# Kernel tuning notes

Measured on AMD Instinct MI355X. Metric: run time of the kernel, lower is better.

## Reference

```python
import jax, jax.numpy as jnp
import numpy as np

NEG = -1e30  # safe -inf surrogate (avoids nan grads through where)
NUM_CLASSES = 128
BLANK = NUM_CLASSES - 1
B, T, L = 256, 512, 64


def setup_inputs() -> dict:
    key = jax.random.key(0)
    k1, k2, k3, k4 = jax.random.split(key, 4)
    y_pred = jax.random.normal(k1, (B, T, NUM_CLASSES), dtype=jnp.float32)
    y_true = jax.random.randint(k2, (B, L), 0, BLANK, dtype=jnp.int32)  # labels in [0, C-2]
    input_length = jax.random.randint(k3, (B,), T // 2, T + 1, dtype=jnp.int32)
    label_length = jax.random.randint(k4, (B,), L // 2, L + 1, dtype=jnp.int32)
    return {"y_true": y_true, "y_pred": y_pred,
            "input_length": input_length, "label_length": label_length}


def ctc_loss(y_pred, y_true, input_length, label_length):
    # y_pred: [B,T,C] logits (batch-major), y_true: [B,L] int labels, blank = C-1.
    Bs, Ts, C = y_pred.shape
    Ls = y_true.shape[1]
    S = 2 * Ls + 1  # extended label lattice: blank, l1, blank, l2, ..., blank
    lp = jax.nn.log_softmax(y_pred.astype(jnp.float32), axis=-1)  # [B,T,C]
    z = jnp.full((Bs, S), BLANK, dtype=jnp.int32).at[:, 1::2].set(y_true)  # [B,S]
    idx = jnp.broadcast_to(z[:, None, :], (Bs, Ts, S))
    lp_z = jnp.take_along_axis(lp, idx, axis=2)  # [B,T,S] log p(z_s | t)
    # skip transition s-2 -> s allowed when z_s is a label differing from z_{s-2}
    s_idx = jnp.arange(S)
    z_m2 = jnp.pad(z[:, :-2], ((0, 0), (2, 0)), constant_values=BLANK)
    skip = (s_idx[None, :] >= 2) & (z != BLANK) & (z != z_m2)  # [B,S]
    alpha0 = (jnp.full((Bs, S), NEG, jnp.float32)
              .at[:, 0].set(lp_z[:, 0, 0])
              .at[:, 1].set(lp_z[:, 0, 1]))
    lps = jnp.moveaxis(lp_z[:, 1:, :], 1, 0)  # [T-1, B, S]
    ts = jnp.arange(1, Ts)

    def step(alpha, xs):
        t, lpt = xs
        a1 = jnp.pad(alpha[:, :-1], ((0, 0), (1, 0)), constant_values=NEG)
        a2 = jnp.where(skip, jnp.pad(alpha[:, :-2], ((0, 0), (2, 0)), constant_values=NEG), NEG)
        new = jnp.logaddexp(jnp.logaddexp(alpha, a1), a2) + lpt
        # freeze rows whose sequence already ended (t >= input_length)
        alpha = jnp.where((t < input_length)[:, None], new, alpha)
        return alpha, None

    alphaT, _ = jax.lax.scan(step, alpha0, (ts, lps))
    e1 = (2 * label_length)[:, None]  # final blank position per row
    a_end = jnp.take_along_axis(alphaT, e1, axis=1)[:, 0]
    a_end2 = jnp.take_along_axis(alphaT, e1 - 1, axis=1)[:, 0]
    return -jnp.logaddexp(a_end, a_end2)  # [B] negative log-likelihood


def reference(y_true, y_pred, input_length, label_length):
    # tf.nn.ctc_loss(labels, logits, label_length, logit_length,
    #                logits_time_major=False, blank_index=num_classes-1)
    return ctc_loss(y_pred, y_true, input_length, label_length)
```

## Files before the change

kernel.cpp:

```cpp
#include <hip/hip_runtime.h>
#include <hip/hip_fp16.h>
#include <math.h>


constexpr int Cc = 128;
constexpr int Tt = 512;
constexpr int Ll = 64;
constexpr int NCH = Tt / 8;
constexpr int NPW = 15;
constexpr int NR  = (NCH + NPW - 1) / NPW;
constexpr float INV_LN2 = 1.4426950408889634f;
constexpr float LN2_F   = 0.6931471805599453f;

__device__ __forceinline__ float fexp2(float x) { return __builtin_amdgcn_exp2f(x); }
__device__ __forceinline__ float flog2(float x) { return __builtin_amdgcn_logf(x); }

template<int CTRL, bool BC>
__device__ __forceinline__ float dppf(float old, float x) {
    return __int_as_float(__builtin_amdgcn_update_dpp(
        __float_as_int(old), __float_as_int(x), CTRL, 0xF, 0xF, BC));
}
__device__ __forceinline__ float wshr1(float x, float fill) { return dppf<0x138, false>(fill, x); }

__device__ __forceinline__ float rlf(float v, int lane) {
    return __int_as_float(__builtin_amdgcn_readlane(__float_as_int(v), lane));
}
__device__ __forceinline__ float rowsum(float e) {
    e += dppf<0x111, true>(0.f, e);
    e += dppf<0x112, true>(0.f, e);
    e += dppf<0x114, true>(0.f, e);
    e += dppf<0x118, true>(0.f, e);
    return e;
}
__device__ __forceinline__ float rowmax(float m) {
    m = fmaxf(m, dppf<0x111, true>(0.f, m));
    m = fmaxf(m, dppf<0x112, true>(0.f, m));
    m = fmaxf(m, dppf<0x114, true>(0.f, m));
    m = fmaxf(m, dppf<0x118, true>(0.f, m));
    return m;
}
__device__ __forceinline__ float allmax(float m) {
    m = rowmax(m);
    return fmaxf(fmaxf(rlf(m, 15), rlf(m, 31)), fmaxf(rlf(m, 47), rlf(m, 63)));
}
__device__ __forceinline__ float bperm_f(int srclane, float v) {
    return __int_as_float(__builtin_amdgcn_ds_bpermute(srclane << 2, __float_as_int(v)));
}
__device__ __forceinline__ float gather4(float4 v, int srclane, int csel) {
    const float gx = bperm_f(srclane, v.x), gy = bperm_f(srclane, v.y);
    const float gz = bperm_f(srclane, v.z), gw = bperm_f(srclane, v.w);
    const float lo = (csel & 1) ? gy : gx;
    const float hi = (csel & 1) ? gw : gz;
    return (csel & 2) ? hi : lo;
}

template<bool GUARD>
__device__ __forceinline__ void do_chunk(uint4 raw, int t0, int inlen, float skf,
                                         float& aO, float& aE, float& r0, float& Rtot)
{
    float dv[8];
    {
        const __half2 h0 = *reinterpret_cast<const __half2*>(&raw.x);
        const __half2 h1 = *reinterpret_cast<const __half2*>(&raw.y);
        const __half2 h2 = *reinterpret_cast<const __half2*>(&raw.z);
        const __half2 h3 = *reinterpret_cast<const __half2*>(&raw.w);
        dv[0] = __low2float(h0); dv[1] = __high2float(h0);
        dv[2] = __low2float(h1); dv[3] = __high2float(h1);
        dv[4] = __low2float(h2); dv[5] = __high2float(h2);
        dv[6] = __low2float(h3); dv[7] = __high2float(h3);
    }
    float sd[8];
#pragma unroll
    for (int j = 0; j < 8; ++j) sd[j] = skf * dv[j];
#pragma unroll
    for (int j = 0; j < 8; ++j) {
        if (!GUARD || (t0 + j < inlen)) {
            const float ad = aO * dv[j];
            const float pE = wshr1(aE, r0);
            const float pO = wshr1(aO, 0.0f);
            const float nO = fmaf(pE, dv[j], fmaf(pO, sd[j], ad));
            aE += aO;
            aO = nO;
        }
    }
    const float M_ = allmax(fmaxf(fmaxf(aO, aE), r0));
    int R_ = (int)(__float_as_uint(M_) >> 23) - 127;
    R_ = (R_ < 0) ? 0 : ((R_ > 126) ? 126 : R_);
    const float sc = __uint_as_float((unsigned)(127 - R_) << 23);
    aO = fminf(aO * sc, 4.0f);
    aE = fminf(aE * sc, 4.0f);
    r0 = fminf(r0 * sc, 4.0f);
    Rtot += (float)R_;
}

__global__ __launch_bounds__(1024, 1) void ctc_fused4_kernel(
    const int* __restrict__ y_true,
    const float* __restrict__ y_pred,
    const int* __restrict__ in_len,
    const int* __restrict__ lab_len,
    float* __restrict__ out)
{
    __shared__ __half w_lds[NCH][64][8];
    __shared__ float  ps[NPW];
    __shared__ int    rctr[NR];

    const int b   = blockIdx.x;
    const int tid = threadIdx.x;
    const int w   = tid >> 6;
    const int l   = tid & 63;

    if (tid < NR) rctr[tid] = 0;
    __syncthreads();

    int inlen = in_len[b]; if (inlen < 1) inlen = 1; if (inlen > Tt) inlen = Tt;
    int LLv   = lab_len[b]; if (LLv < 1) LLv = 1; if (LLv > Ll) LLv = Ll;

    const int lab = y_true[b * Ll + l] & 127;
    const float* rowbase = y_pred + (size_t)b * Tt * Cc;

    if (w != 0) {
        const int pw   = w - 1;
        const int half = l >> 5, li = l & 31;
        const int srcA = lab >> 2;
        const int csel = lab & 3;
        const bool live = (l < LLv);

        float acc = 0.0f;

        float4 vb[4];
#pragma unroll
        for (int j = 0; j < 4; ++j)
            vb[j] = ((const float4*)(rowbase + (size_t)(pw * 8 + 2 * j + half) * Cc))[li];

        int r = 0;
        for (int c = pw; c < NCH; c += NPW, ++r) {
            const int cn = (c + NPW < NCH) ? (c + NPW) : (NCH - 1);
            float prod = 1.0f, bsum = 0.0f;
#pragma unroll
            for (int j = 0; j < 4; ++j) {
                const float4 v = vb[j];
                vb[j] = ((const float4*)(rowbase + (size_t)(cn * 8 + 2 * j + half) * Cc))[li];

                const int rA = c * 8 + 2 * j;
                const int rB = rA + 1;

                float e = (fexp2(v.x * INV_LN2) + fexp2(v.y * INV_LN2))
                        + (fexp2(v.z * INV_LN2) + fexp2(v.w * INV_LN2));
                e = rowsum(e);
                const float sA = rlf(e, 15) + rlf(e, 31);
                const float sB = rlf(e, 47) + rlf(e, 63);
                const float blA = rlf(v.w, 31);
                const float blB = rlf(v.w, 63);

                const bool okA = rA < inlen, okB = rB < inlen;
                prod *= okB ? sA * sB : (okA ? sA : 1.0f);
                bsum += okB ? blA + blB : (okA ? blA : 0.0f);

                const float xA = gather4(v, srcA, csel);
                const float xB = gather4(v, srcA + 32, csel);
                float wA = fminf(fmaxf(fexp2((xA - blA) * INV_LN2), 6.1e-5f), 8192.0f);
                float wB = fminf(fmaxf(fexp2((xB - blB) * INV_LN2), 6.1e-5f), 8192.0f);
                wA = live ? wA : 0.0f;
                wB = live ? wB : 0.0f;
                const unsigned packed =
                      (unsigned)__half_as_ushort(__float2half(wA))
                    | ((unsigned)__half_as_ushort(__float2half(wB)) << 16);
                *(unsigned*)&w_lds[c][l][2 * j] = packed;
            }
            acc = fmaf(bsum, INV_LN2, acc) - flog2(prod);
            if (c + NPW >= NCH && l == 0) ps[pw] = acc;
            asm volatile("s_waitcnt lgkmcnt(0)" ::: "memory");
            if (l == 0) atomicAdd(&rctr[r], 1);
        }
        return;
    }

    const int labp = __shfl_up(lab, 1, 64);
    const float skf = ((l >= 1) && (lab != labp)) ? 1.0f : 0.0f;

    float aO = 0.0f, aE = 0.0f, r0 = 1.0f, Rtot = 0.0f;
    const int nchunks = (inlen + 7) >> 3;

    volatile int* vctr = rctr;
    int ready = 0, rr = 0;
    auto wait_upto = [&](int cneed) {
        while (ready <= cneed) {
            const int rem  = NCH - rr * NPW;
            const int need = rem < NPW ? rem : NPW;
            if (vctr[rr] >= need) { ready += need; ++rr; }
            else __builtin_amdgcn_s_sleep(1);
        }
        asm volatile("" ::: "memory");
    };

    wait_upto(0);
    uint4 A = *(const uint4*)&w_lds[0][l][0];
    for (int c = 0; c < nchunks; ++c) {
        uint4 Bv = A;
        if (c + 1 < nchunks) {
            wait_upto(c + 1);
            Bv = *(const uint4*)&w_lds[c + 1][l][0];
        }
        const int t0 = c * 8;
        if (t0 + 8 <= inlen) do_chunk<false>(A, t0, inlen, skf, aO, aE, r0, Rtot);
        else                 do_chunk<true >(A, t0, inlen, skf, aO, aE, r0, Rtot);
        A = Bv;
    }

    while (rr < NR) {
        const int rem  = NCH - rr * NPW;
        const int need = rem < NPW ? rem : NPW;
        if (vctr[rr] >= need) ++rr;
        else __builtin_amdgcn_s_sleep(1);
    }
    asm volatile("" ::: "memory");

    float cum_b = 0.0f;
#pragma unroll
    for (int q = 0; q < NPW; ++q) cum_b += ps[q];

    const float aEr = __shfl(aE, LLv - 1, 64);
    const float aOr = __shfl(aO, LLv - 1, 64);
    if (l == 0)
        out[b] = -LN2_F * (flog2(fmaxf(aEr + aOr, 1e-37f)) + Rtot + cum_b);
}

extern "C" void kernel_launch(void* const* d_in, const int* in_sizes, int n_in,
                              void* d_out, int out_size, void* d_ws, size_t ws_size,
                              hipStream_t stream) {
    const int*   y_true  = (const int*)d_in[0];
    const float* y_pred  = (const float*)d_in[1];
    const int*   in_len  = (const int*)d_in[2];
    const int*   lab_len = (const int*)d_in[3];
    float*       out     = (float*)d_out;
    (void)d_ws; (void)ws_size;

    ctc_fused4_kernel<<<256, 1024, 0, stream>>>(y_true, y_pred, in_len, lab_len, out);
}
```

Before: 111.7 us.

## Split CTC recursion into concurrent forward-alpha and backward-beta halves meeting mid-sequence

The serial alpha recursion over all time chunks is replaced by two waves: one runs the forward recursion over the first half of the chunks and another runs a backward beta recursion over the second half. The two meet in the middle through a dot product of alpha and beta, reduced in double precision. Producer waves are split into two groups of seven that fill the emission weights from both ends, so each consumer gets data in the order it needs. This roughly halves the serial dependency chain, at the cost of extra synchronisation, a double-precision reduction, and a separate scaling scheme for the backward pass.

```diff
diff --git a/kernel.cpp b/kernel.cpp
--- a/kernel.cpp
+++ b/kernel.cpp
@@ -6,9 +6,7 @@
 constexpr int Cc = 128;
 constexpr int Tt = 512;
 constexpr int Ll = 64;
-constexpr int NCH = Tt / 8;
-constexpr int NPW = 15;
-constexpr int NR  = (NCH + NPW - 1) / NPW;
+constexpr int NPS = 7;
 constexpr float INV_LN2 = 1.4426950408889634f;
 constexpr float LN2_F   = 0.6931471805599453f;
 
@@ -21,6 +19,7 @@
         __float_as_int(old), __float_as_int(x), CTRL, 0xF, 0xF, BC));
 }
 __device__ __forceinline__ float wshr1(float x, float fill) { return dppf<0x138, false>(fill, x); }
+__device__ __forceinline__ float wshl1(float x, float fill) { return dppf<0x130, false>(fill, x); }
 
 __device__ __forceinline__ float rlf(float v, int lane) {
     return __int_as_float(__builtin_amdgcn_readlane(__float_as_int(v), lane));
@@ -53,22 +52,30 @@
     const float hi = (csel & 1) ? gw : gz;
     return (csel & 2) ? hi : lo;
 }
+__device__ __forceinline__ double shflx_d(double v, int mask) {
+    const long long x = __double_as_longlong(v);
+    int lo = (int)(x & 0xffffffffLL), hi = (int)(x >> 32);
+    lo = __shfl_xor(lo, mask, 64);
+    hi = __shfl_xor(hi, mask, 64);
+    return __longlong_as_double(((long long)hi << 32) | (unsigned)(unsigned int)lo);
+}
+
+__device__ __forceinline__ void unpack8(uint4 raw, float (&dv)[8]) {
+    const __half2 h0 = *reinterpret_cast<const __half2*>(&raw.x);
+    const __half2 h1 = *reinterpret_cast<const __half2*>(&raw.y);
+    const __half2 h2 = *reinterpret_cast<const __half2*>(&raw.z);
+    const __half2 h3 = *reinterpret_cast<const __half2*>(&raw.w);
+    dv[0] = __low2float(h0); dv[1] = __high2float(h0);
+    dv[2] = __low2float(h1); dv[3] = __high2float(h1);
+    dv[4] = __low2float(h2); dv[5] = __high2float(h2);
+    dv[6] = __low2float(h3); dv[7] = __high2float(h3);
+}
 
 template<bool GUARD>
 __device__ __forceinline__ void do_chunk(uint4 raw, int t0, int inlen, float skf,
                                          float& aO, float& aE, float& r0, float& Rtot)
 {
-    float dv[8];
-    {
-        const __half2 h0 = *reinterpret_cast<const __half2*>(&raw.x);
-        const __half2 h1 = *reinterpret_cast<const __half2*>(&raw.y);
-        const __half2 h2 = *reinterpret_cast<const __half2*>(&raw.z);
-        const __half2 h3 = *reinterpret_cast<const __half2*>(&raw.w);
-        dv[0] = __low2float(h0); dv[1] = __high2float(h0);
-        dv[2] = __low2float(h1); dv[3] = __high2float(h1);
-        dv[4] = __low2float(h2); dv[5] = __high2float(h2);
-        dv[6] = __low2float(h3); dv[7] = __high2float(h3);
-    }
+    float dv[8]; unpack8(raw, dv);
     float sd[8];
 #pragma unroll
     for (int j = 0; j < 8; ++j) sd[j] = skf * dv[j];
@@ -93,136 +100,226 @@
     Rtot += (float)R_;
 }
 
-__global__ __launch_bounds__(1024, 1) void ctc_fused4_kernel(
+template<bool GUARD>
+__device__ __forceinline__ void do_chunk_bwd(uint4 raw, int t0, int inlen, float skfb,
+                                             float& bO, float& bE, float& br, float& Rb,
+                                             int l)
+{
+    float dv[8]; unpack8(raw, dv);
+#pragma unroll
+    for (int j = 7; j >= 0; --j) {
+        if (!GUARD || (t0 + j < inlen)) {
+            const float BOw = bO * dv[j];
+            const float uO  = wshl1(BOw, 0.0f);
+            const float t1  = bE + BOw;
+            bE += uO;
+            br += BOw;
+            bO  = fmaf(skfb, uO, t1);
+        }
+    }
+    const float brm = (l == 0) ? br : 0.0f;
+    const float M_ = allmax(fmaxf(fmaxf(bO, bE), brm));
+    int R_ = (int)(__float_as_uint(M_) >> 23) - 127;
+    R_ = (R_ < 0) ? 0 : ((R_ > 126) ? 126 : R_);
+    const float sc = __uint_as_float((unsigned)(127 - R_) << 23);
+    bO = fminf(bO * sc, 4.0f);
+    bE = fminf(bE * sc, 4.0f);
+    br = fminf(br * sc, 4.0f);
+    Rb += (float)R_;
+}
+
+__global__ __launch_bounds__(1024, 1) void ctc_fused7_kernel(
     const int* __restrict__ y_true,
     const float* __restrict__ y_pred,
     const int* __restrict__ in_len,
     const int* __restrict__ lab_len,
     float* __restrict__ out)
 {
-    __shared__ __half w_lds[NCH][64][8];
-    __shared__ float  ps[NPW];
-    __shared__ int    rctr[NR];
+    __shared__ __half w_lds[Tt / 8][64][8];
+    __shared__ float  ps[2 * NPS];
+    __shared__ int    fctr[5], bctr[5];
+    __shared__ int    bdone, pdone;
+    __shared__ float  bstate[130];
 
     const int b   = blockIdx.x;
     const int tid = threadIdx.x;
     const int w   = tid >> 6;
     const int l   = tid & 63;
 
-    if (tid < NR) rctr[tid] = 0;
+    if (tid < 5) { fctr[tid] = 0; bctr[tid] = 0; }
+    if (tid == 0) { bdone = 0; pdone = 0; }
     __syncthreads();
 
     int inlen = in_len[b]; if (inlen < 1) inlen = 1; if (inlen > Tt) inlen = Tt;
     int LLv   = lab_len[b]; if (LLv < 1) LLv = 1; if (LLv > Ll) LLv = Ll;
 
+    const int nct  = (inlen + 7) >> 3;
+    const int nchf = nct >> 1;
+    const int nchb = nct - nchf;
+
     const int lab = y_true[b * Ll + l] & 127;
     const float* rowbase = y_pred + (size_t)b * Tt * Cc;
 
-    if (w != 0) {
-        const int pw   = w - 1;
+    if (w >= 2) {
+        const bool asc = (w < 9);
+        const int pw    = asc ? (w - 2) : (w - 9);
+        const int nside = asc ? nchf : nchb;
         const int half = l >> 5, li = l & 31;
         const int srcA = lab >> 2;
         const int csel = lab & 3;
         const bool live = (l < LLv);
+        int* ctr = asc ? fctr : bctr;
 
         float acc = 0.0f;
 
-        float4 vb[4];
-#pragma unroll
-        for (int j = 0; j < 4; ++j)
-            vb[j] = ((const float4*)(rowbase + (size_t)(pw * 8 + 2 * j + half) * Cc))[li];
-
-        int r = 0;
-        for (int c = pw; c < NCH; c += NPW, ++r) {
-            const int cn = (c + NPW < NCH) ? (c + NPW) : (NCH - 1);
-            float prod = 1.0f, bsum = 0.0f;
-#pragma unroll
-            for (int j = 0; j < 4; ++j) {
-                const float4 v = vb[j];
-                vb[j] = ((const float4*)(rowbase + (size_t)(cn * 8 + 2 * j + half) * Cc))[li];
-
-                const int rA = c * 8 + 2 * j;
-                const int rB = rA + 1;
-
-                float e = (fexp2(v.x * INV_LN2) + fexp2(v.y * INV_LN2))
-                        + (fexp2(v.z * INV_LN2) + fexp2(v.w * INV_LN2));
-                e = rowsum(e);
-                const float sA = rlf(e, 15) + rlf(e, 31);
-                const float sB = rlf(e, 47) + rlf(e, 63);
-                const float blA = rlf(v.w, 31);
-                const float blB = rlf(v.w, 63);
-
-                const bool okA = rA < inlen, okB = rB < inlen;
-                prod *= okB ? sA * sB : (okA ? sA : 1.0f);
-                bsum += okB ? blA + blB : (okA ? blA : 0.0f);
-
-                const float xA = gather4(v, srcA, csel);
-                const float xB = gather4(v, srcA + 32, csel);
-                float wA = fminf(fmaxf(fexp2((xA - blA) * INV_LN2), 6.1e-5f), 8192.0f);
-                float wB = fminf(fmaxf(fexp2((xB - blB) * INV_LN2), 6.1e-5f), 8192.0f);
-                wA = live ? wA : 0.0f;
-                wB = live ? wB : 0.0f;
-                const unsigned packed =
-                      (unsigned)__half_as_ushort(__float2half(wA))
-                    | ((unsigned)__half_as_ushort(__float2half(wB)) << 16);
-                *(unsigned*)&w_lds[c][l][2 * j] = packed;
+        if (pw < nside) {
+            const int c0 = asc ? pw : (nct - 1 - pw);
+            float4 vb[4];
+#pragma unroll
+            for (int j = 0; j < 4; ++j)
+                vb[j] = ((const float4*)(rowbase + (size_t)(c0 * 8 + 2 * j + half) * Cc))[li];
+
+            for (int k = pw, idx = 0; k < nside; k += NPS, ++idx) {
+                const int c  = asc ? k : (nct - 1 - k);
+                const int kn = k + NPS;
+                const int cn = (kn < nside) ? (asc ? kn : (nct - 1 - kn)) : 0;
+                float prod = 1.0f, bsum = 0.0f;
+#pragma unroll
+                for (int j = 0; j < 4; ++j) {
+                    const float4 v = vb[j];
+                    vb[j] = ((const float4*)(rowbase + (size_t)(cn * 8 + 2 * j + half) * Cc))[li];
+
+                    const int rA = c * 8 + 2 * j;
+                    const int rB = rA + 1;
+
+                    float e = (fexp2(v.x * INV_LN2) + fexp2(v.y * INV_LN2))
+                            + (fexp2(v.z * INV_LN2) + fexp2(v.w * INV_LN2));
+                    e = rowsum(e);
+                    const float sA = rlf(e, 15) + rlf(e, 31);
+                    const float sB = rlf(e, 47) + rlf(e, 63);
+                    const float blA = rlf(v.w, 31);
+                    const float blB = rlf(v.w, 63);
+
+                    const bool okA = rA < inlen, okB = rB < inlen;
+                    prod *= okB ? sA * sB : (okA ? sA : 1.0f);
+                    bsum += okB ? blA + blB : (okA ? blA : 0.0f);
+
+                    const float xA = gather4(v, srcA, csel);
+                    const float xB = gather4(v, srcA + 32, csel);
+                    float wA = fminf(fmaxf(fexp2((xA - blA) * INV_LN2), 6.1e-5f), 8192.0f);
+                    float wB = fminf(fmaxf(fexp2((xB - blB) * INV_LN2), 6.1e-5f), 8192.0f);
+                    wA = live ? wA : 0.0f;
+                    wB = live ? wB : 0.0f;
+                    const unsigned packed =
+                          (unsigned)__half_as_ushort(__float2half(wA))
+                        | ((unsigned)__half_as_ushort(__float2half(wB)) << 16);
+                    *(unsigned*)&w_lds[c][l][2 * j] = packed;
+                }
+                acc = fmaf(bsum, INV_LN2, acc) - flog2(prod);
+                asm volatile("s_waitcnt lgkmcnt(0)" ::: "memory");
+                if (l == 0) atomicAdd(&ctr[idx], 1);
             }
-            acc = fmaf(bsum, INV_LN2, acc) - flog2(prod);
-            if (c + NPW >= NCH && l == 0) ps[pw] = acc;
-            asm volatile("s_waitcnt lgkmcnt(0)" ::: "memory");
-            if (l == 0) atomicAdd(&rctr[r], 1);
-        }
+        }
+        if (l == 0) ps[(asc ? 0 : NPS) + pw] = acc;
+        asm volatile("s_waitcnt lgkmcnt(0)" ::: "memory");
+        if (l == 0) atomicAdd(&pdone, 1);
         return;
     }
 
     const int labp = __shfl_up(lab, 1, 64);
     const float skf = ((l >= 1) && (lab != labp)) ? 1.0f : 0.0f;
 
-    float aO = 0.0f, aE = 0.0f, r0 = 1.0f, Rtot = 0.0f;
-    const int nchunks = (inlen + 7) >> 3;
-
-    volatile int* vctr = rctr;
-    int ready = 0, rr = 0;
-    auto wait_upto = [&](int cneed) {
-        while (ready <= cneed) {
-            const int rem  = NCH - rr * NPW;
-            const int need = rem < NPW ? rem : NPW;
-            if (vctr[rr] >= need) { ready += need; ++rr; }
+    if (w == 1) {
+        const float skfb = __shfl(skf, (l + 1) & 63, 64);
+        float bE = (l == LLv - 1) ? 1.0f : 0.0f;
+        float bO = bE;
+        float br = 0.0f, Rb = 0.0f;
+
+        volatile int* vd = bctr;
+        int readyd = 0, rrd = 0;
+        auto wait_d = [&](int cb) {
+            const int needcnt = nct - cb;
+            while (readyd < needcnt) {
+                const int rem  = nchb - rrd * NPS;
+                const int need = rem < NPS ? rem : NPS;
+                if (vd[rrd] >= need) { readyd += need; ++rrd; }
+                else __builtin_amdgcn_s_sleep(1);
+            }
+            asm volatile("" ::: "memory");
+        };
+
+        if (nchb > 0) {
+            wait_d(nct - 1);
+            uint4 A = *(const uint4*)&w_lds[nct - 1][l][0];
+            for (int cb = nct - 1; cb >= nchf; --cb) {
+                uint4 Bv = A;
+                if (cb - 1 >= nchf) { wait_d(cb - 1); Bv = *(const uint4*)&w_lds[cb - 1][l][0]; }
+                const int t0 = cb * 8;
+                if (t0 + 8 <= inlen) do_chunk_bwd<false>(A, t0, inlen, skfb, bO, bE, br, Rb, l);
+                else                 do_chunk_bwd<true >(A, t0, inlen, skfb, bO, bE, br, Rb, l);
+                A = Bv;
+            }
+        }
+        bstate[l]      = bE;
+        bstate[64 + l] = bO;
+        if (l == 0) { bstate[128] = br; bstate[129] = Rb; }
+        asm volatile("s_waitcnt lgkmcnt(0)" ::: "memory");
+        if (l == 0) atomicExch(&bdone, 1);
+        return;
+    }
+
+    float aO = 0.0f, aE = 0.0f, r0 = 1.0f, Rf = 0.0f;
+
+    volatile int* vf = fctr;
+    int readyf = 0, rrf = 0;
+    auto wait_f = [&](int cneed) {
+        while (readyf <= cneed) {
+            const int rem  = nchf - rrf * NPS;
+            const int need = rem < NPS ? rem : NPS;
+            if (vf[rrf] >= need) { readyf += need; ++rrf; }
             else __builtin_amdgcn_s_sleep(1);
         }
         asm volatile("" ::: "memory");
     };
 
-    wait_upto(0);
-    uint4 A = *(const uint4*)&w_lds[0][l][0];
-    for (int c = 0; c < nchunks; ++c) {
-        uint4 Bv = A;
-        if (c + 1 < nchunks) {
-            wait_upto(c + 1);
-            Bv = *(const uint4*)&w_lds[c + 1][l][0];
-        }
-        const int t0 = c * 8;
-        if (t0 + 8 <= inlen) do_chunk<false>(A, t0, inlen, skf, aO, aE, r0, Rtot);
-        else                 do_chunk<true >(A, t0, inlen, skf, aO, aE, r0, Rtot);
-        A = Bv;
-    }
-
-    while (rr < NR) {
-        const int rem  = NCH - rr * NPW;
-        const int need = rem < NPW ? rem : NPW;
-        if (vctr[rr] >= need) ++rr;
-        else __builtin_amdgcn_s_sleep(1);
-    }
-    asm volatile("" ::: "memory");
+    if (nchf > 0) {
+        wait_f(0);
+        uint4 A = *(const uint4*)&w_lds[0][l][0];
+        for (int c = 0; c < nchf; ++c) {
+            uint4 Bv = A;
+            if (c + 1 < nchf) { wait_f(c + 1); Bv = *(const uint4*)&w_lds[c + 1][l][0]; }
+            const int t0 = c * 8;
+            if (t0 + 8 <= inlen) do_chunk<false>(A, t0, inlen, skf, aO, aE, r0, Rf);
+            else                 do_chunk<true >(A, t0, inlen, skf, aO, aE, r0, Rf);
+            A = Bv;
+        }
+    }
+
+    {
+        volatile int* vp = &pdone;
+        while (*vp < 2 * NPS) __builtin_amdgcn_s_sleep(1);
+        volatile int* vbd = &bdone;
+        while (*vbd == 0) __builtin_amdgcn_s_sleep(1);
+        asm volatile("" ::: "memory");
+    }
 
     float cum_b = 0.0f;
 #pragma unroll
-    for (int q = 0; q < NPW; ++q) cum_b += ps[q];
-
-    const float aEr = __shfl(aE, LLv - 1, 64);
-    const float aOr = __shfl(aO, LLv - 1, 64);
+    for (int q = 0; q < 2 * NPS; ++q) cum_b += ps[q];
+
+    const float bEl = bstate[l], bOl = bstate[64 + l];
+    const float br0 = bstate[128], Rb = bstate[129];
+    double cd = (double)aE * (double)bEl + (double)aO * (double)bOl;
+    if (l == 0) cd += (double)r0 * (double)br0;
+#pragma unroll
+    for (int mk = 1; mk < 64; mk <<= 1) cd += shflx_d(cd, mk);
+    double sd_ = cd > 1e-300 ? cd : 1e-300;
+    const long long u = __double_as_longlong(sd_);
+    const int e2 = (int)((u >> 52) & 0x7ff) - 1023;
+    const double mant = __longlong_as_double((u & 0xfffffffffffffLL) | 0x3ff0000000000000LL);
+    const float l2s = (float)e2 + flog2((float)mant);
     if (l == 0)
-        out[b] = -LN2_F * (flog2(fmaxf(aEr + aOr, 1e-37f)) + Rtot + cum_b);
+        out[b] = -LN2_F * (l2s + Rf + Rb + cum_b);
 }
 
 extern "C" void kernel_launch(void* const* d_in, const int* in_sizes, int n_in,
@@ -235,5 +332,5 @@
     float*       out     = (float*)d_out;
     (void)d_ws; (void)ws_size;
 
-    ctc_fused4_kernel<<<256, 1024, 0, stream>>>(y_true, y_pred, in_len, lab_len, out);
-}
+    ctc_fused7_kernel<<<256, 1024, 0, stream>>>(y_true, y_pred, in_len, lab_len, out);
+}
```

Result: no change. 109.7 us (-1.8%).
